# Optimization experiments

Hardware: AMD Instinct MI355X
Metric: run time of the kernel (lower is better)

Reference implementation:

```python
import jax, jax.numpy as jnp
import numpy as np
from jax import lax

B, S, DM = 4, 4096, 1024
H, P, R = 16, 32, 8
D = DM // H  # head_dim = 64
K_SEL = 4


def setup_inputs() -> dict:
    key = jax.random.key(0)
    ks = jax.random.split(key, 6)
    x = jax.random.normal(ks[0], (B, S, DM), dtype=jnp.float32)
    K_state = jax.random.normal(ks[1], (H, P, R, D), dtype=jnp.float32) / np.sqrt(D)
    V_state = jax.random.normal(ks[2], (H, P, R, D), dtype=jnp.float32) / np.sqrt(D)
    W_router = jax.random.normal(ks[3], (H, D, P), dtype=jnp.float32) / np.sqrt(D)
    W_out = jax.random.normal(ks[4], (DM, DM), dtype=jnp.float32) / np.sqrt(DM)
    b_out = jnp.zeros((DM,), dtype=jnp.float32)
    return {"x": x, "K_state": K_state, "V_state": V_state,
            "W_router": W_router, "W_out": W_out, "b_out": b_out, "k": K_SEL}


def reference(x, K_state, V_state, W_router, W_out, b_out, k):
    b, s, dm = x.shape
    h, p, r, d = K_state.shape
    xh = x.reshape(b, s, h, d)  # per-head token features

    # Router: top-k partition selection per token per head.
    logits = jnp.einsum('bshd,hdp->bshp', xh, W_router)
    topv = lax.top_k(logits, k)[0]            # [b,s,h,k]
    thresh = topv[..., -1:]                   # k-th largest logit
    neg_inf = jnp.array(-jnp.inf, dtype=logits.dtype)
    gates = jax.nn.softmax(jnp.where(logits >= thresh, logits, neg_inf), axis=-1)  # [b,s,h,p], zero off top-k

    # Attention over state rows within each partition (masked-dense == sparse gather math).
    scale = jnp.asarray(1.0 / np.sqrt(d), dtype=x.dtype)
    scores = jnp.einsum('bshd,hprd->bshpr', xh, K_state) * scale
    attn = jax.nn.softmax(scores, axis=-1)    # softmax over rows r within a partition

    # Gate-weighted combine of per-partition attention outputs, fused to avoid [b,s,h,p,d].
    w = attn * gates[..., None]               # [b,s,h,p,r]
    heads = jnp.einsum('bshpr,hprd->bshd', w, V_state)

    out = heads.reshape(b, s, dm) @ W_out + b_out
    return out
```

## Files before the change

kernel.cpp:

```cpp
#include <hip/hip_runtime.h>
#include <hip/hip_bf16.h>

#define BB 4
#define SS 4096
#define DM 1024
#define HH 16
#define PP 32
#define RR 8
#define DD 64
#define NTOK (BB*SS)
#define MM NTOK
#define NN DM
#define KK DM

typedef __attribute__((ext_vector_type(8))) short short8;
typedef __attribute__((ext_vector_type(4))) float floatx4;

static __device__ inline short f2bf(float f) {
    union { __hip_bfloat16 b; short s; } u; u.b = __float2bfloat16(f); return u.s;
}
static __device__ inline short8 pack8(float4 lo, float4 hi) {
    short8 r;
    r[0] = f2bf(lo.x); r[1] = f2bf(lo.y); r[2] = f2bf(lo.z); r[3] = f2bf(lo.w);
    r[4] = f2bf(hi.x); r[5] = f2bf(hi.y); r[6] = f2bf(hi.z); r[7] = f2bf(hi.w);
    return r;
}

static __device__ inline unsigned bfr(float f) {
    unsigned u = __float_as_uint(f);
    return u + 0x7fffu + ((u >> 16) & 1u);
}
static __device__ inline int pk2(float a, float b) {
    return __builtin_amdgcn_perm(bfr(b), bfr(a), 0x07060302);
}
static __device__ inline short8 pk8(float4 lo, float4 hi) {
    union { short8 s; int i[4]; } r;
    r.i[0] = pk2(lo.x, lo.y); r.i[1] = pk2(lo.z, lo.w);
    r.i[2] = pk2(hi.x, hi.y); r.i[3] = pk2(hi.z, hi.w);
    return r.s;
}

__global__ __launch_bounds__(256) void convert_w(const float* __restrict__ Wo,
                                                 __hip_bfloat16* __restrict__ wsw) {
    int tid = blockIdx.x * 256 + threadIdx.x;
    int l = tid & 63;
    int kblk = (tid >> 6) & 31;
    int ntile = tid >> 11;
    int col = ntile * 16 + (l & 15);
    int krow = kblk * 32 + (l >> 4) * 8;
#pragma unroll
    for (int j = 0; j < 8; ++j) {
        wsw[(size_t)tid * 8 + j] = __float2bfloat16(Wo[(size_t)(krow + j) * NN + col]);
    }
}

__global__ __launch_bounds__(256) void convert_kv(const float* __restrict__ Kst,
                                                  const float* __restrict__ Vst,
                                                  __hip_bfloat16* __restrict__ kfrag,
                                                  __hip_bfloat16* __restrict__ vfrag) {
    int tid = blockIdx.x * 256 + threadIdx.x;
    int arr = tid >> 15;
    int idx = tid & 32767;
    int h = idx >> 11, blk = (idx >> 6) & 31, fl = idx & 63;
    int fm = fl & 15, fk = fl >> 4;
    short8 val;
    short* dst;
    if (arr == 0) {
        int mt = blk >> 1, kb = blk & 1;
        int pr = mt * 16 + fm, d0 = kb * 32 + fk * 8;
        const float* src = Kst + ((size_t)h * 256 + pr) * 64 + d0;
        float4 lo = *(const float4*)src, hi = *(const float4*)(src + 4);
        val = pack8(lo, hi);
        dst = (short*)kfrag + (size_t)idx * 8;
    } else {
        int mt = blk >> 3, kb = blk & 7;
        int d = mt * 16 + fm, pr0 = kb * 32 + fk * 8;
        const float* src = Vst + ((size_t)h * 256 + pr0) * 64 + d;
#pragma unroll
        for (int j = 0; j < 8; ++j) val[j] = f2bf(src[j * 64]);
        dst = (short*)vfrag + (size_t)idx * 8;
    }
    *(short8*)dst = val;
}

__global__ __launch_bounds__(256, 3) void attn_v7(const float* __restrict__ x,
                                                  const float* __restrict__ Wr,
                                                  const __hip_bfloat16* __restrict__ kfrag,
                                                  const __hip_bfloat16* __restrict__ vfrag,
                                                  const int* __restrict__ kp,
                                                  __hip_bfloat16* __restrict__ hb) {
    __shared__ __align__(16) char smem[40960];
    float (*xs)[68]     = (float (*)[68])smem;
    float (*Lg)[36]     = (float (*)[36])(smem + 17408);
    short* wf           = (short*)smem;
    float (*gatesT)[64] = (float (*)[64])(smem + 32768);

    const int lane = threadIdx.x & 63;
    const int w = threadIdx.x >> 6;
    const int l15 = lane & 15, l4 = lane >> 4;
    const int t0 = blockIdx.x * 64;
    const int h = blockIdx.y;

    {
        int row = threadIdx.x >> 2, q = threadIdx.x & 3;
        const float4* src = (const float4*)(x + (size_t)(t0 + row) * DM + h * 64 + q * 16);
        float4 v0 = src[0], v1 = src[1], v2 = src[2], v3 = src[3];
        float4* dst = (float4*)&xs[row][q * 16];
        dst[0] = v0; dst[1] = v1; dst[2] = v2; dst[3] = v3;
    }

    const int p = lane & 31, dh = lane >> 5;
    float wreg[32];
    {
        const float* wrp = Wr + (size_t)h * (DD * PP) + dh * 32 * PP + p;
#pragma unroll
        for (int dd = 0; dd < 32; ++dd) wreg[dd] = wrp[dd * PP];
    }
    const int kkv = kp[0];

    short8 xb[4][2];
#pragma unroll
    for (int nt = 0; nt < 4; ++nt)
#pragma unroll
        for (int kb = 0; kb < 2; ++kb) {
            const float* bp = x + (size_t)(t0 + nt * 16 + l15) * DM + h * 64 + kb * 32 + l4 * 8;
            float4 lo = *(const float4*)bp;
            float4 hi = *(const float4*)(bp + 4);
            xb[nt][kb] = pk8(lo, hi);
        }
    short8 ka[4][2];
#pragma unroll
    for (int mi = 0; mi < 4; ++mi)
#pragma unroll
        for (int kb = 0; kb < 2; ++kb)
            ka[mi][kb] = *(const short8*)((const short*)kfrag +
                          ((size_t)(h * 32 + (w * 4 + mi) * 2 + kb) * 512 + lane * 8));

    __syncthreads();

    floatx4 acc[4][4] = {};
#pragma unroll
    for (int kb = 0; kb < 2; ++kb)
#pragma unroll
        for (int mi = 0; mi < 4; ++mi)
#pragma unroll
            for (int nt = 0; nt < 4; ++nt)
                acc[mi][nt] = __builtin_amdgcn_mfma_f32_16x16x32_bf16(ka[mi][kb], xb[nt][kb], acc[mi][nt], 0, 0, 0);

    for (int it = 0; it < 16; it += 2) {
        const int ta = w * 16 + it;
        const int tb = ta + 1;
        float la = 0.f, lb = 0.f;
#pragma unroll
        for (int j = 0; j < 8; ++j) {
            float4 qa = *(const float4*)&xs[ta][dh * 32 + 4 * j];
            float4 qb = *(const float4*)&xs[tb][dh * 32 + 4 * j];
            la += qa.x * wreg[4 * j];     lb += qb.x * wreg[4 * j];
            la += qa.y * wreg[4 * j + 1]; lb += qb.y * wreg[4 * j + 1];
            la += qa.z * wreg[4 * j + 2]; lb += qb.z * wreg[4 * j + 2];
            la += qa.w * wreg[4 * j + 3]; lb += qb.w * wreg[4 * j + 3];
        }
        la += __shfl_xor(la, 32);
        lb += __shfl_xor(lb, 32);
        if (lane < 32) {
            Lg[ta][lane] = la;
            Lg[tb][lane] = lb;
        }
    }
    __syncthreads();

    float thresh = 0.f, a1 = 0.f;
    if (lane < 16) {
        int t = w * 16 + lane;
        float lgr[32];
        const float4* lrow = (const float4*)&Lg[t][0];
#pragma unroll
        for (int c = 0; c < 8; ++c) {
            float4 q4 = lrow[c];
            lgr[4 * c] = q4.x; lgr[4 * c + 1] = q4.y; lgr[4 * c + 2] = q4.z; lgr[4 * c + 3] = q4.w;
        }
        float aa = -INFINITY, b2 = -INFINITY, c3 = -INFINITY, d4 = -INFINITY;
#pragma unroll
        for (int pp = 0; pp < 32; ++pp) {
            float v = lgr[pp];
            float na = fmaxf(aa, v); v = fminf(aa, v); aa = na;
            float nb = fmaxf(b2, v); v = fminf(b2, v); b2 = nb;
            float nc = fmaxf(c3, v); v = fminf(c3, v); c3 = nc;
            d4 = fmaxf(d4, v);
        }
        thresh = (kkv >= 4) ? d4 : (kkv == 3 ? c3 : (kkv == 2 ? b2 : aa));
        a1 = aa;
    }
    thresh = __shfl(thresh, l15);
    a1     = __shfl(a1, l15);

    {
        const int t = w * 16 + l15;
        const int p8 = l4 * 8;
        const float4* lrow = (const float4*)&Lg[t][p8];
        float4 qa = lrow[0], qb = lrow[1];
        float e0 = (qa.x >= thresh) ? __expf(qa.x - a1) : 0.f;
        float e1 = (qa.y >= thresh) ? __expf(qa.y - a1) : 0.f;
        float e2 = (qa.z >= thresh) ? __expf(qa.z - a1) : 0.f;
        float e3 = (qa.w >= thresh) ? __expf(qa.w - a1) : 0.f;
        float e4 = (qb.x >= thresh) ? __expf(qb.x - a1) : 0.f;
        float e5 = (qb.y >= thresh) ? __expf(qb.y - a1) : 0.f;
        float e6 = (qb.z >= thresh) ? __expf(qb.z - a1) : 0.f;
        float e7 = (qb.w >= thresh) ? __expf(qb.w - a1) : 0.f;
        float part = ((e0 + e1) + (e2 + e3)) + ((e4 + e5) + (e6 + e7));
        part += __shfl_xor(part, 16);
        part += __shfl_xor(part, 32);
        float inv = 1.f / part;
        gatesT[p8 + 0][t] = e0 * inv;
        gatesT[p8 + 1][t] = e1 * inv;
        gatesT[p8 + 2][t] = e2 * inv;
        gatesT[p8 + 3][t] = e3 * inv;
        gatesT[p8 + 4][t] = e4 * inv;
        gatesT[p8 + 5][t] = e5 * inv;
        gatesT[p8 + 6][t] = e6 * inv;
        gatesT[p8 + 7][t] = e7 * inv;
    }
    __syncthreads();

#pragma unroll
    for (int mi = 0; mi < 4; ++mi) {
        const int mt = w * 4 + mi;
        const int pidx = mt * 2 + (l4 >> 1);
#pragma unroll
        for (int nt = 0; nt < 4; ++nt) {
            float g = gatesT[pidx][nt * 16 + l15];
            float s0 = acc[mi][nt][0] * 0.125f;
            float s1 = acc[mi][nt][1] * 0.125f;
            float s2 = acc[mi][nt][2] * 0.125f;
            float s3 = acc[mi][nt][3] * 0.125f;
            float mx = fmaxf(fmaxf(s0, s1), fmaxf(s2, s3));
            mx = fmaxf(mx, __shfl_xor(mx, 16));
            float e0 = __expf(s0 - mx), e1 = __expf(s1 - mx);
            float e2 = __expf(s2 - mx), e3 = __expf(s3 - mx);
            float loc = (e0 + e1) + (e2 + e3);
            float se = loc + __shfl_xor(loc, 16);
            float ws = g / se;
            int2 pk;
            pk.x = pk2(e0 * ws, e1 * ws);
            pk.y = pk2(e2 * ws, e3 * ws);
            int off = (((mt & 1) * 2 + (l4 >> 1)) * 16 + l15) * 8 + (l4 & 1) * 4;
            *(int2*)&wf[(nt * 8 + (mt >> 1)) * 512 + off] = pk;
        }
    }
    __syncthreads();

    floatx4 h4[4] = {};
#pragma unroll
    for (int kb = 0; kb < 8; ++kb) {
        short8 va = *(const short8*)((const short*)vfrag +
                      ((size_t)(h * 32 + w * 8 + kb) * 512 + lane * 8));
#pragma unroll
        for (int nt = 0; nt < 4; ++nt) {
            short8 wb = *(const short8*)&wf[(nt * 8 + kb) * 512 + lane * 8];
            h4[nt] = __builtin_amdgcn_mfma_f32_16x16x32_bf16(va, wb, h4[nt], 0, 0, 0);
        }
    }
#pragma unroll
    for (int nt = 0; nt < 4; ++nt) {
        int t = t0 + nt * 16 + l15;
        int2 pk;
        pk.x = pk2(h4[nt][0], h4[nt][1]);
        pk.y = pk2(h4[nt][2], h4[nt][3]);
        *(int2*)((short*)hb + (size_t)t * DM + h * 64 + w * 16 + l4 * 4) = pk;
    }
}

__global__ __launch_bounds__(256) void gemm_v5(const __hip_bfloat16* __restrict__ Abf,
                                               const __hip_bfloat16* __restrict__ Bsw,
                                               const float* __restrict__ bias,
                                               float* __restrict__ C) {
    __shared__ __align__(16) short As[2][8192];
    const int lane = threadIdx.x & 63;
    const int wave = threadIdx.x >> 6;
    const int wm = wave >> 1, wn = wave & 1;

    const int wg  = blockIdx.y * 8 + blockIdx.x;
    const int xcd = wg & 7;
    const int loc = wg >> 3;
    const int bm0 = (xcd * 16 + (loc >> 3)) * 128;
    const int bn0 = (loc & 7) * 128;

    const int l15 = lane & 15, l4 = lane >> 4;

    const short* Ap = (const short*)Abf;
    const short* Bp = (const short*)Bsw;

    int crow[4], ck8[4];
#pragma unroll
    for (int j = 0; j < 4; ++j) {
        int c = (wave * 4 + j) * 64 + lane;
        int row = c >> 3;
        crow[j] = row;
        ck8[j] = ((c & 7) ^ (row & 7)) * 8;
    }

    int boff[4];
#pragma unroll
    for (int nt = 0; nt < 4; ++nt)
        boff[nt] = (((bn0 >> 4) + wn * 4 + nt) * 32) * 512 + lane * 8;

    const int axor = l15 & 7;
    int arow[4];
#pragma unroll
    for (int mt = 0; mt < 4; ++mt)
        arow[mt] = (wm * 64 + mt * 16 + l15) * 64;
    const int ak0 = (l4 ^ axor) * 8;
    const int ak1 = ((4 + l4) ^ axor) * 8;

    floatx4 acc[4][4] = {};

#pragma unroll
    for (int j = 0; j < 4; ++j)
        __builtin_amdgcn_global_load_lds(
            (const __attribute__((address_space(1))) unsigned int*)
                (Ap + (size_t)(bm0 + crow[j]) * KK + ck8[j]),
            (__attribute__((address_space(3))) unsigned int*)&As[0][(wave * 4 + j) * 512],
            16, 0, 0);
    short8 bA[4];
#pragma unroll
    for (int nt = 0; nt < 4; ++nt)
        bA[nt] = *(const short8*)(Bp + boff[nt]);
    __syncthreads();

    for (int step = 0; step < 16; ++step) {
        const int cur = step & 1;
        const int nxt = cur ^ 1;

        short8 bB[4];
#pragma unroll
        for (int nt = 0; nt < 4; ++nt)
            bB[nt] = *(const short8*)(Bp + boff[nt] + (size_t)(2 * step + 1) * 512);

        if (step < 15) {
#pragma unroll
            for (int j = 0; j < 4; ++j)
                __builtin_amdgcn_global_load_lds(
                    (const __attribute__((address_space(1))) unsigned int*)
                        (Ap + (size_t)(bm0 + crow[j]) * KK + (step + 1) * 64 + ck8[j]),
                    (__attribute__((address_space(3))) unsigned int*)&As[nxt][(wave * 4 + j) * 512],
                    16, 0, 0);
        }

        short8 a0[4];
#pragma unroll
        for (int mt = 0; mt < 4; ++mt)
            a0[mt] = *(const short8*)&As[cur][arow[mt] + ak0];
#pragma unroll
        for (int mt = 0; mt < 4; ++mt)
#pragma unroll
            for (int nt = 0; nt < 4; ++nt)
                acc[mt][nt] = __builtin_amdgcn_mfma_f32_16x16x32_bf16(a0[mt], bA[nt], acc[mt][nt], 0, 0, 0);

        short8 a1[4];
#pragma unroll
        for (int mt = 0; mt < 4; ++mt)
            a1[mt] = *(const short8*)&As[cur][arow[mt] + ak1];
#pragma unroll
        for (int mt = 0; mt < 4; ++mt)
#pragma unroll
            for (int nt = 0; nt < 4; ++nt)
                acc[mt][nt] = __builtin_amdgcn_mfma_f32_16x16x32_bf16(a1[mt], bB[nt], acc[mt][nt], 0, 0, 0);

        if (step < 15) {
#pragma unroll
            for (int nt = 0; nt < 4; ++nt)
                bA[nt] = *(const short8*)(Bp + boff[nt] + (size_t)(2 * step + 2) * 512);
        }
        __syncthreads();
    }

#pragma unroll
    for (int nt = 0; nt < 4; ++nt) {
        const int col = bn0 + wn * 64 + nt * 16 + l15;
        const float bv = bias[col];
#pragma unroll
        for (int mt = 0; mt < 4; ++mt) {
            const int row0 = bm0 + wm * 64 + mt * 16 + l4 * 4;
#pragma unroll
            for (int i = 0; i < 4; ++i)
                C[(size_t)(row0 + i) * NN + col] = acc[mt][nt][i] + bv;
        }
    }
}

extern "C" void kernel_launch(void* const* d_in, const int* in_sizes, int n_in,
                              void* d_out, int out_size, void* d_ws, size_t ws_size,
                              hipStream_t stream) {
    const float* x   = (const float*)d_in[0];
    const float* Kst = (const float*)d_in[1];
    const float* Vst = (const float*)d_in[2];
    const float* Wr  = (const float*)d_in[3];
    const float* Wo  = (const float*)d_in[4];
    const float* bo  = (const float*)d_in[5];
    const int*   kp  = (const int*)d_in[6];
    float* out = (float*)d_out;

    __hip_bfloat16* hb    = (__hip_bfloat16*)d_ws;
    __hip_bfloat16* wsw   = hb + (size_t)MM * KK;
    __hip_bfloat16* kfrag = wsw + (size_t)KK * NN;
    __hip_bfloat16* vfrag = kfrag + 16 * 32 * 512;

    convert_w<<<dim3(512), 256, 0, stream>>>(Wo, wsw);
    convert_kv<<<dim3(256), 256, 0, stream>>>(Kst, Vst, kfrag, vfrag);
    attn_v7<<<dim3(NTOK / 64, HH), 256, 0, stream>>>(x, Wr, kfrag, vfrag, kp, hb);
    gemm_v5<<<dim3(NN / 128, MM / 128), 256, 0, stream>>>(hb, wsw, bo, out);
}
```

Before: 245.4 us.

## Split router gating into separate kernel and merge conversion kernels

Merges the weight and K/V conversion kernels into one launch, and splits the fused attention kernel into a router/gating kernel that writes gates to global memory plus an MFMA attention kernel that reads them. The aim is to lower register and shared-memory pressure in each kernel and remove the mid-kernel synchronization between gating and score computation. In exchange it adds a global round trip for the gates (about 8 MB written and read), reads x twice, and adds an extra launch.

```diff
diff --git a/kernel.cpp b/kernel.cpp
--- a/kernel.cpp
+++ b/kernel.cpp
@@ -40,60 +40,57 @@
     return r.s;
 }
 
-__global__ __launch_bounds__(256) void convert_w(const float* __restrict__ Wo,
-                                                 __hip_bfloat16* __restrict__ wsw) {
-    int tid = blockIdx.x * 256 + threadIdx.x;
-    int l = tid & 63;
-    int kblk = (tid >> 6) & 31;
-    int ntile = tid >> 11;
-    int col = ntile * 16 + (l & 15);
-    int krow = kblk * 32 + (l >> 4) * 8;
-#pragma unroll
-    for (int j = 0; j < 8; ++j) {
-        wsw[(size_t)tid * 8 + j] = __float2bfloat16(Wo[(size_t)(krow + j) * NN + col]);
-    }
-}
-
-__global__ __launch_bounds__(256) void convert_kv(const float* __restrict__ Kst,
-                                                  const float* __restrict__ Vst,
-                                                  __hip_bfloat16* __restrict__ kfrag,
-                                                  __hip_bfloat16* __restrict__ vfrag) {
-    int tid = blockIdx.x * 256 + threadIdx.x;
-    int arr = tid >> 15;
-    int idx = tid & 32767;
-    int h = idx >> 11, blk = (idx >> 6) & 31, fl = idx & 63;
-    int fm = fl & 15, fk = fl >> 4;
-    short8 val;
-    short* dst;
-    if (arr == 0) {
-        int mt = blk >> 1, kb = blk & 1;
-        int pr = mt * 16 + fm, d0 = kb * 32 + fk * 8;
-        const float* src = Kst + ((size_t)h * 256 + pr) * 64 + d0;
-        float4 lo = *(const float4*)src, hi = *(const float4*)(src + 4);
-        val = pack8(lo, hi);
-        dst = (short*)kfrag + (size_t)idx * 8;
+__global__ __launch_bounds__(256) void convert_all(const float* __restrict__ Wo,
+                                                   const float* __restrict__ Kst,
+                                                   const float* __restrict__ Vst,
+                                                   __hip_bfloat16* __restrict__ wsw,
+                                                   __hip_bfloat16* __restrict__ kfrag,
+                                                   __hip_bfloat16* __restrict__ vfrag) {
+    if (blockIdx.x < 512) {
+        int tid = blockIdx.x * 256 + threadIdx.x;
+        int l = tid & 63;
+        int kblk = (tid >> 6) & 31;
+        int ntile = tid >> 11;
+        int col = ntile * 16 + (l & 15);
+        int krow = kblk * 32 + (l >> 4) * 8;
+#pragma unroll
+        for (int j = 0; j < 8; ++j) {
+            wsw[(size_t)tid * 8 + j] = __float2bfloat16(Wo[(size_t)(krow + j) * NN + col]);
+        }
     } else {
-        int mt = blk >> 3, kb = blk & 7;
-        int d = mt * 16 + fm, pr0 = kb * 32 + fk * 8;
-        const float* src = Vst + ((size_t)h * 256 + pr0) * 64 + d;
-#pragma unroll
-        for (int j = 0; j < 8; ++j) val[j] = f2bf(src[j * 64]);
-        dst = (short*)vfrag + (size_t)idx * 8;
-    }
-    *(short8*)dst = val;
-}
-
-__global__ __launch_bounds__(256, 3) void attn_v7(const float* __restrict__ x,
-                                                  const float* __restrict__ Wr,
-                                                  const __hip_bfloat16* __restrict__ kfrag,
-                                                  const __hip_bfloat16* __restrict__ vfrag,
-                                                  const int* __restrict__ kp,
-                                                  __hip_bfloat16* __restrict__ hb) {
-    __shared__ __align__(16) char smem[40960];
-    float (*xs)[68]     = (float (*)[68])smem;
-    float (*Lg)[36]     = (float (*)[36])(smem + 17408);
-    short* wf           = (short*)smem;
-    float (*gatesT)[64] = (float (*)[64])(smem + 32768);
+        int tid = (blockIdx.x - 512) * 256 + threadIdx.x;
+        int arr = tid >> 15;
+        int idx = tid & 32767;
+        int h = idx >> 11, blk = (idx >> 6) & 31, fl = idx & 63;
+        int fm = fl & 15, fk = fl >> 4;
+        short8 val;
+        short* dst;
+        if (arr == 0) {
+            int mt = blk >> 1, kb = blk & 1;
+            int pr = mt * 16 + fm, d0 = kb * 32 + fk * 8;
+            const float* src = Kst + ((size_t)h * 256 + pr) * 64 + d0;
+            float4 lo = *(const float4*)src, hi = *(const float4*)(src + 4);
+            val = pack8(lo, hi);
+            dst = (short*)kfrag + (size_t)idx * 8;
+        } else {
+            int mt = blk >> 3, kb = blk & 7;
+            int d = mt * 16 + fm, pr0 = kb * 32 + fk * 8;
+            const float* src = Vst + ((size_t)h * 256 + pr0) * 64 + d;
+#pragma unroll
+            for (int j = 0; j < 8; ++j) val[j] = f2bf(src[j * 64]);
+            dst = (short*)vfrag + (size_t)idx * 8;
+        }
+        *(short8*)dst = val;
+    }
+}
+
+__global__ __launch_bounds__(256) void router_gates(const float* __restrict__ x,
+                                                    const float* __restrict__ Wr,
+                                                    const int* __restrict__ kp,
+                                                    float* __restrict__ gates_g) {
+    __shared__ __align__(16) char smem[26624];
+    float (*xs)[68] = (float (*)[68])smem;
+    float (*Lg)[36] = (float (*)[36])(smem + 17408);
 
     const int lane = threadIdx.x & 63;
     const int w = threadIdx.x >> 6;
@@ -118,34 +115,7 @@
     }
     const int kkv = kp[0];
 
-    short8 xb[4][2];
-#pragma unroll
-    for (int nt = 0; nt < 4; ++nt)
-#pragma unroll
-        for (int kb = 0; kb < 2; ++kb) {
-            const float* bp = x + (size_t)(t0 + nt * 16 + l15) * DM + h * 64 + kb * 32 + l4 * 8;
-            float4 lo = *(const float4*)bp;
-            float4 hi = *(const float4*)(bp + 4);
-            xb[nt][kb] = pk8(lo, hi);
-        }
-    short8 ka[4][2];
-#pragma unroll
-    for (int mi = 0; mi < 4; ++mi)
-#pragma unroll
-        for (int kb = 0; kb < 2; ++kb)
-            ka[mi][kb] = *(const short8*)((const short*)kfrag +
-                          ((size_t)(h * 32 + (w * 4 + mi) * 2 + kb) * 512 + lane * 8));
-
     __syncthreads();
-
-    floatx4 acc[4][4] = {};
-#pragma unroll
-    for (int kb = 0; kb < 2; ++kb)
-#pragma unroll
-        for (int mi = 0; mi < 4; ++mi)
-#pragma unroll
-            for (int nt = 0; nt < 4; ++nt)
-                acc[mi][nt] = __builtin_amdgcn_mfma_f32_16x16x32_bf16(ka[mi][kb], xb[nt][kb], acc[mi][nt], 0, 0, 0);
 
     for (int it = 0; it < 16; it += 2) {
         const int ta = w * 16 + it;
@@ -211,24 +181,74 @@
         part += __shfl_xor(part, 16);
         part += __shfl_xor(part, 32);
         float inv = 1.f / part;
-        gatesT[p8 + 0][t] = e0 * inv;
-        gatesT[p8 + 1][t] = e1 * inv;
-        gatesT[p8 + 2][t] = e2 * inv;
-        gatesT[p8 + 3][t] = e3 * inv;
-        gatesT[p8 + 4][t] = e4 * inv;
-        gatesT[p8 + 5][t] = e5 * inv;
-        gatesT[p8 + 6][t] = e6 * inv;
-        gatesT[p8 + 7][t] = e7 * inv;
-    }
-    __syncthreads();
+        float* gb = gates_g + ((size_t)(h * (NTOK / 64) + blockIdx.x) * 32) * 64 + t;
+        gb[(p8 + 0) * 64] = e0 * inv;
+        gb[(p8 + 1) * 64] = e1 * inv;
+        gb[(p8 + 2) * 64] = e2 * inv;
+        gb[(p8 + 3) * 64] = e3 * inv;
+        gb[(p8 + 4) * 64] = e4 * inv;
+        gb[(p8 + 5) * 64] = e5 * inv;
+        gb[(p8 + 6) * 64] = e6 * inv;
+        gb[(p8 + 7) * 64] = e7 * inv;
+    }
+}
+
+__global__ __launch_bounds__(256, 3) void attn_mm(const float* __restrict__ x,
+                                                  const __hip_bfloat16* __restrict__ kfrag,
+                                                  const __hip_bfloat16* __restrict__ vfrag,
+                                                  const float* __restrict__ gates_g,
+                                                  __hip_bfloat16* __restrict__ hb) {
+    __shared__ __align__(16) short wf[16384];
+
+    const int lane = threadIdx.x & 63;
+    const int w = threadIdx.x >> 6;
+    const int l15 = lane & 15, l4 = lane >> 4;
+    const int t0 = blockIdx.x * 64;
+    const int h = blockIdx.y;
+
+    const float* gb = gates_g + ((size_t)(h * (NTOK / 64) + blockIdx.x) * 32) * 64;
+    float gv[4][4];
+#pragma unroll
+    for (int mi = 0; mi < 4; ++mi) {
+        const int pidx = (w * 4 + mi) * 2 + (l4 >> 1);
+#pragma unroll
+        for (int nt = 0; nt < 4; ++nt)
+            gv[mi][nt] = gb[pidx * 64 + nt * 16 + l15];
+    }
+
+    short8 xb[4][2];
+#pragma unroll
+    for (int nt = 0; nt < 4; ++nt)
+#pragma unroll
+        for (int kb = 0; kb < 2; ++kb) {
+            const float* bp = x + (size_t)(t0 + nt * 16 + l15) * DM + h * 64 + kb * 32 + l4 * 8;
+            float4 lo = *(const float4*)bp;
+            float4 hi = *(const float4*)(bp + 4);
+            xb[nt][kb] = pk8(lo, hi);
+        }
+    short8 ka[4][2];
+#pragma unroll
+    for (int mi = 0; mi < 4; ++mi)
+#pragma unroll
+        for (int kb = 0; kb < 2; ++kb)
+            ka[mi][kb] = *(const short8*)((const short*)kfrag +
+                          ((size_t)(h * 32 + (w * 4 + mi) * 2 + kb) * 512 + lane * 8));
+
+    floatx4 acc[4][4] = {};
+#pragma unroll
+    for (int kb = 0; kb < 2; ++kb)
+#pragma unroll
+        for (int mi = 0; mi < 4; ++mi)
+#pragma unroll
+            for (int nt = 0; nt < 4; ++nt)
+                acc[mi][nt] = __builtin_amdgcn_mfma_f32_16x16x32_bf16(ka[mi][kb], xb[nt][kb], acc[mi][nt], 0, 0, 0);
 
 #pragma unroll
     for (int mi = 0; mi < 4; ++mi) {
         const int mt = w * 4 + mi;
-        const int pidx = mt * 2 + (l4 >> 1);
 #pragma unroll
         for (int nt = 0; nt < 4; ++nt) {
-            float g = gatesT[pidx][nt * 16 + l15];
+            float g = gv[mi][nt];
             float s0 = acc[mi][nt][0] * 0.125f;
             float s1 = acc[mi][nt][1] * 0.125f;
             float s2 = acc[mi][nt][2] * 0.125f;
@@ -404,9 +424,10 @@
     __hip_bfloat16* wsw   = hb + (size_t)MM * KK;
     __hip_bfloat16* kfrag = wsw + (size_t)KK * NN;
     __hip_bfloat16* vfrag = kfrag + 16 * 32 * 512;
-
-    convert_w<<<dim3(512), 256, 0, stream>>>(Wo, wsw);
-    convert_kv<<<dim3(256), 256, 0, stream>>>(Kst, Vst, kfrag, vfrag);
-    attn_v7<<<dim3(NTOK / 64, HH), 256, 0, stream>>>(x, Wr, kfrag, vfrag, kp, hb);
+    float* gates_g = (float*)(vfrag + 16 * 32 * 512);
+
+    convert_all<<<dim3(768), 256, 0, stream>>>(Wo, Kst, Vst, wsw, kfrag, vfrag);
+    router_gates<<<dim3(NTOK / 64, HH), 256, 0, stream>>>(x, Wr, kp, gates_g);
+    attn_mm<<<dim3(NTOK / 64, HH), 256, 0, stream>>>(x, kfrag, vfrag, gates_g, hb);
     gemm_v5<<<dim3(NN / 128, MM / 128), 256, 0, stream>>>(hb, wsw, bo, out);
 }
```

After: 241.7 us. No clear change (-1.5%).
